# Performance work log

Hardware: AMD Instinct MI355X
Metric: run time of the kernel (lower is better)

Reference implementation:

```python
import jax, jax.numpy as jnp
import numpy as np

KERNEL_MUL = 2.0
KERNEL_NUM = 5


def setup_inputs() -> dict:
    key = jax.random.key(0)
    k1, k2 = jax.random.split(key)
    N, D = 4096, 256
    source = jax.random.normal(k1, (N, D), dtype=jnp.float32)
    target = jax.random.normal(k2, (N, D), dtype=jnp.float32)
    return {"source": source, "target": target}


def _gaussian_kernel_sum(source, target):
    # total: [2N, D]
    total = jnp.concatenate([source, target], axis=0)
    n = total.shape[0]
    sq = jnp.sum(total * total, axis=1)  # [2N]
    L2 = sq[:, None] + sq[None, :] - 2.0 * (total @ total.T)  # [2N, 2N]
    # Bandwidth from detached mean of off-diagonal-normalized sum (torch uses .data)
    bandwidth = jax.lax.stop_gradient(jnp.sum(L2)) / (n * n - n)
    bandwidth = bandwidth / (KERNEL_MUL ** (KERNEL_NUM // 2))
    kernels = sum(
        jnp.exp(-L2 / (bandwidth * (KERNEL_MUL ** i))) for i in range(KERNEL_NUM)
    )
    return kernels


def reference(source, target):
    b = source.shape[0]
    K = _gaussian_kernel_sum(source, target)
    XX = jnp.mean(K[:b, :b])
    YY = jnp.mean(K[b:, b:])
    XY = jnp.mean(K[:b, b:])
    YX = jnp.mean(K[b:, :b])
    return XX + YY - XY - YX
```

## Files before the change

kernel.cpp:

```cpp
#include <hip/hip_runtime.h>


#define NROWS 8192
#define HALF  4096
#define DIM   256
#define BM    128
#define CONVB 256
#define NTILE 2080

typedef __bf16 bf16x8 __attribute__((ext_vector_type(8)));
typedef float f32x4 __attribute__((ext_vector_type(4)));
typedef unsigned short ushort8 __attribute__((ext_vector_type(8)));

__device__ __forceinline__ const float* row_ptr(const float* src, const float* tgt, int r) {
    return (r < HALF) ? (src + (size_t)r * DIM) : (tgt + (size_t)(r - HALF) * DIM);
}

__device__ __forceinline__ unsigned short bf16_rne(float x) {
    unsigned int u = __builtin_bit_cast(unsigned int, x);
    return (unsigned short)((u + 0x7FFFu + ((u >> 16) & 1u)) >> 16);
}

__global__ __launch_bounds__(256) void k_conv(const float* __restrict__ src,
                                              const float* __restrict__ tgt,
                                              unsigned short* __restrict__ hi,
                                              float* __restrict__ sq,
                                              float* __restrict__ part,
                                              double* __restrict__ parts1,
                                              double* __restrict__ accum) {
    __shared__ __align__(16) unsigned short sh_hi[32 * 32 * 8];
    __shared__ float4 cs[4][64];
    __shared__ double s1s[4];

    int w = threadIdx.x >> 6, lane = threadIdx.x & 63;
    int r0 = blockIdx.x * 32;
    int g  = lane >> 1, j = lane & 1;
    float4 csum = {0.f, 0.f, 0.f, 0.f};
    double s1w = 0.0;
    #pragma unroll
    for (int i = 0; i < 8; ++i) {
        int rl  = w * 8 + i;
        int row = r0 + rl;
        const float* rp = row_ptr(src, tgt, row);
        float4 v = ((const float4*)rp)[lane];
        float xs[4] = {v.x, v.y, v.z, v.w};
        unsigned short hs[4];
        #pragma unroll
        for (int k = 0; k < 4; ++k) hs[k] = bf16_rne(xs[k]);
        ushort4 h4 = {hs[0], hs[1], hs[2], hs[3]};
        int so = (g * 32 + rl) * 8 + j * 4;
        *(ushort4*)&sh_hi[so] = h4;
        csum.x += v.x; csum.y += v.y; csum.z += v.z; csum.w += v.w;
        float s = v.x * v.x + v.y * v.y + v.z * v.z + v.w * v.w;
        #pragma unroll
        for (int off = 32; off; off >>= 1) s += __shfl_xor(s, off, 64);
        if (lane == 0) { sq[row] = s; s1w += (double)s; }
    }
    __syncthreads();
    int panel = blockIdx.x >> 2, quarter = blockIdx.x & 3;
    #pragma unroll
    for (int c = threadIdx.x; c < 1024; c += 256) {
        int gg = c >> 5, r = c & 31;
        size_t goff = (((size_t)panel * 32 + gg) * 128 + quarter * 32 + r) * 8;
        *(ushort8*)&hi[goff] = *(const ushort8*)&sh_hi[c * 8];
    }
    cs[w][lane] = csum;
    if (lane == 0) s1s[w] = s1w;
    __syncthreads();
    if (w == 0) {
        float4 a = cs[0][lane], b = cs[1][lane], c = cs[2][lane], d = cs[3][lane];
        float4 tot = {a.x + b.x + c.x + d.x, a.y + b.y + c.y + d.y,
                      a.z + b.z + c.z + d.z, a.w + b.w + c.w + d.w};
        *(float4*)&part[(size_t)blockIdx.x * DIM + lane * 4] = tot;
        if (lane == 0) parts1[blockIdx.x] = s1s[0] + s1s[1] + s1s[2] + s1s[3];
    }
    if (blockIdx.x == 0 && threadIdx.x == 0) *accum = 0.0;
}

__global__ __launch_bounds__(256) void k_scale(const double* __restrict__ parts1,
                                               const float* __restrict__ part,
                                               float* __restrict__ scale) {
    __shared__ double sh[256];
    int t = threadIdx.x;
    sh[t] = parts1[t];
    __syncthreads();
    for (int off = 128; off; off >>= 1) {
        if (t < off) sh[t] += sh[t + off];
        __syncthreads();
    }
    double S1 = sh[0];
    __syncthreads();
    float c0 = 0.f, c1 = 0.f, c2 = 0.f, c3 = 0.f;
    #pragma unroll 16
    for (int b = 0; b < CONVB; b += 4) {
        c0 += part[(b + 0) * DIM + t];
        c1 += part[(b + 1) * DIM + t];
        c2 += part[(b + 2) * DIM + t];
        c3 += part[(b + 3) * DIM + t];
    }
    double c = (double)((c0 + c1) + (c2 + c3));
    sh[t] = c * c;
    __syncthreads();
    for (int off = 128; off; off >>= 1) {
        if (t < off) sh[t] += sh[t + off];
        __syncthreads();
    }
    if (t == 0) {
        double S2    = sh[0];
        double n     = (double)NROWS;
        double sumL2 = 2.0 * n * S1 - 2.0 * S2;
        double bw    = sumL2 / (n * n - n) / 4.0;
        *scale = (float)(-1.0 / (16.0 * bw * 0.69314718055994530942));
    }
}

__global__ __launch_bounds__(256, 2) void k_pairs(const unsigned short* __restrict__ hi,
                                                  const float* __restrict__ sq,
                                                  const float* __restrict__ scale_p,
                                                  double* __restrict__ accum) {
    int gidx = blockIdx.x;
    int I = 0;
    for (;;) {
        int rowcnt = 36 + 64 * (7 - I);
        if (gidx < rowcnt) break;
        gidx -= rowcnt; ++I;
    }
    int bi, bj;
    if (gidx < 36) {
        int r = 0, c = gidx;
        while (c >= 8 - r) { c -= 8 - r; ++r; }
        bi = 8 * I + r; bj = 8 * I + r + c;
    } else {
        int o = gidx - 36;
        int J = I + 1 + (o >> 6);
        int k2 = o & 63;
        bi = 8 * I + (k2 >> 3); bj = 8 * J + (k2 & 7);
    }

    __shared__ float wsum[4];

    int t    = threadIdx.x;
    int lane = t & 63;
    int w    = t >> 6;
    int wr   = w >> 1, wc = w & 1;
    int lr   = lane & 15, lq = lane >> 4;
    int ro = bi * BM, co = bj * BM;

    size_t aBase = (size_t)bi * 4096 + lq * 128 + wr * 64 + lr;
    size_t bBase = (size_t)bj * 4096 + lq * 128 + wc * 64 + lr;
    const ushort8* pAh = (const ushort8*)hi + aBase;
    const ushort8* pBh = (const ushort8*)hi + bBase;

    f32x4 acc[4][4];
    #pragma unroll
    for (int m = 0; m < 4; ++m)
        #pragma unroll
        for (int n = 0; n < 4; ++n) acc[m][n] = (f32x4){0.f, 0.f, 0.f, 0.f};

    #pragma unroll
    for (int it = 0; it < DIM / 128; ++it) {
        bf16x8 aH[4][4], bH[4][4];
        #pragma unroll
        for (int h = 0; h < 4; ++h) {
            #pragma unroll
            for (int m = 0; m < 4; ++m) {
                aH[h][m] = __builtin_bit_cast(bf16x8, pAh[it * 2048 + h * 512 + m * 16]);
                bH[h][m] = __builtin_bit_cast(bf16x8, pBh[it * 2048 + h * 512 + m * 16]);
            }
        }
        #pragma unroll
        for (int h = 0; h < 4; ++h)
            #pragma unroll
            for (int m = 0; m < 4; ++m)
                #pragma unroll
                for (int n = 0; n < 4; ++n)
                    acc[m][n] = __builtin_amdgcn_mfma_f32_16x16x32_bf16(aH[h][m], bH[h][n], acc[m][n], 0, 0, 0);
    }

    float scale = *scale_p;
    int ro_eff = ro + wr * 64, co_eff = co + wc * 64;
    float4 sqa4[4];
    float  sqbv[4];
    #pragma unroll
    for (int m = 0; m < 4; ++m) sqa4[m] = *(const float4*)&sq[ro_eff + m * 16 + lq * 4];
    #pragma unroll
    for (int n = 0; n < 4; ++n) sqbv[n] = sq[co_eff + n * 16 + lr];

    float tsum = 0.0f;
    #pragma unroll
    for (int m = 0; m < 4; ++m) {
        float sa[4] = {sqa4[m].x, sqa4[m].y, sqa4[m].z, sqa4[m].w};
        #pragma unroll
        for (int n = 0; n < 4; ++n) {
            #pragma unroll
            for (int r = 0; r < 4; ++r) {
                float L2  = sa[r] + sqbv[n] - 2.0f * acc[m][n][r];
                float u   = __builtin_amdgcn_exp2f(scale * L2);
                float u2  = u * u;
                float u4  = u2 * u2;
                float u8  = u4 * u4;
                float u16 = u8 * u8;
                tsum += u + u2 + u4 + u8 + u16;
            }
        }
    }

    #pragma unroll
    for (int off = 32; off; off >>= 1) tsum += __shfl_xor(tsum, off, 64);
    if (lane == 0) wsum[w] = tsum;
    __syncthreads();
    if (t == 0) {
        float tot = wsum[0] + wsum[1] + wsum[2] + wsum[3];
        float sgn = ((ro < HALF) == (co < HALF)) ? 1.0f : -1.0f;
        float wgt = (bi == bj) ? 1.0f : 2.0f;
        atomicAdd(accum, (double)(sgn * wgt * tot));
    }
}

__global__ void k_fin(const double* __restrict__ accum, float* __restrict__ out) {
    out[0] = (float)(*accum / ((double)HALF * (double)HALF));
}

extern "C" void kernel_launch(void* const* d_in, const int* in_sizes, int n_in,
                              void* d_out, int out_size, void* d_ws, size_t ws_size,
                              hipStream_t stream) {
    const float* src = (const float*)d_in[0];
    const float* tgt = (const float*)d_in[1];
    float* out = (float*)d_out;

    char* ws = (char*)d_ws;
    double* accum  = (double*)ws;
    float*  scale  = (float*)(ws + 16);
    float*  sq     = (float*)(ws + 64);
    float*  part   = (float*)(ws + 64 + 32768);
    double* parts1 = (double*)(ws + 64 + 32768 + 262144);
    unsigned short* hi = (unsigned short*)(ws + 297024);

    k_conv <<<CONVB, 256, 0, stream>>>(src, tgt, hi, sq, part, parts1, accum);
    k_scale<<<1, 256, 0, stream>>>(parts1, part, scale);
    k_pairs<<<NTILE, 256, 0, stream>>>(hi, sq, scale, accum);
    k_fin  <<<1, 1, 0, stream>>>(accum, out);
}
```

Baseline: 112.7 us.

## Remap pair kernel to 256x128 blocks with per-wave 64x128 tiles

Replaces the 128x128 upper-triangle block tiling (2080 blocks) with blocks covering two 128-row panels against one 128-column panel (1056 blocks). Each wave now computes a 64x128 tile with 32 accumulators and loops over K in 32-wide steps, loading 4 A and 8 B fragments per step. The triangular weighting moves to per-wave weights of 0, 1 or 2, so some waves compute tiles that are then discarded. This aims to raise operand reuse per wave and cut block count, at the cost of more accumulator registers and some wasted work on diagonal blocks.

```diff
diff --git a/kernel.cpp b/kernel.cpp
--- a/kernel.cpp
+++ b/kernel.cpp
@@ -4,9 +4,8 @@
 #define NROWS 8192
 #define HALF  4096
 #define DIM   256
-#define BM    128
 #define CONVB 256
-#define NTILE 2080
+#define NTILE 1056
 
 typedef __bf16 bf16x8 __attribute__((ext_vector_type(8)));
 typedef float f32x4 __attribute__((ext_vector_type(4)));
@@ -118,80 +117,70 @@
                                                   const float* __restrict__ sq,
                                                   const float* __restrict__ scale_p,
                                                   double* __restrict__ accum) {
-    int gidx = blockIdx.x;
+    int id = blockIdx.x;
     int I = 0;
     for (;;) {
-        int rowcnt = 36 + 64 * (7 - I);
-        if (gidx < rowcnt) break;
-        gidx -= rowcnt; ++I;
-    }
-    int bi, bj;
-    if (gidx < 36) {
-        int r = 0, c = gidx;
-        while (c >= 8 - r) { c -= 8 - r; ++r; }
-        bi = 8 * I + r; bj = 8 * I + r + c;
-    } else {
-        int o = gidx - 36;
-        int J = I + 1 + (o >> 6);
-        int k2 = o & 63;
-        bi = 8 * I + (k2 >> 3); bj = 8 * J + (k2 & 7);
-    }
+        int cnt = 64 - 2 * I;
+        if (id < cnt) break;
+        id -= cnt; ++I;
+    }
+    int J = 2 * I + id;
 
     __shared__ float wsum[4];
 
     int t    = threadIdx.x;
     int lane = t & 63;
     int w    = t >> 6;
-    int wr   = w >> 1, wc = w & 1;
     int lr   = lane & 15, lq = lane >> 4;
-    int ro = bi * BM, co = bj * BM;
-
-    size_t aBase = (size_t)bi * 4096 + lq * 128 + wr * 64 + lr;
-    size_t bBase = (size_t)bj * 4096 + lq * 128 + wc * 64 + lr;
+    int Pw   = 2 * I + (w >> 1);
+    int hh   = w & 1;
+
+    float wgt = (J == Pw) ? 1.0f : (J > Pw) ? 2.0f : 0.0f;
+    float sgn = ((Pw < 32) == (J < 32)) ? 1.0f : -1.0f;
+
+    size_t aBase = (size_t)Pw * 4096 + lq * 128 + hh * 64 + lr;
+    size_t bBase = (size_t)J  * 4096 + lq * 128 + lr;
     const ushort8* pAh = (const ushort8*)hi + aBase;
     const ushort8* pBh = (const ushort8*)hi + bBase;
 
-    f32x4 acc[4][4];
+    f32x4 acc[4][8];
     #pragma unroll
     for (int m = 0; m < 4; ++m)
         #pragma unroll
-        for (int n = 0; n < 4; ++n) acc[m][n] = (f32x4){0.f, 0.f, 0.f, 0.f};
-
-    #pragma unroll
-    for (int it = 0; it < DIM / 128; ++it) {
-        bf16x8 aH[4][4], bH[4][4];
-        #pragma unroll
-        for (int h = 0; h < 4; ++h) {
+        for (int n = 0; n < 8; ++n) acc[m][n] = (f32x4){0.f, 0.f, 0.f, 0.f};
+
+    #pragma unroll
+    for (int it = 0; it < DIM / 32; ++it) {
+        bf16x8 aH[4], bH[8];
+        #pragma unroll
+        for (int m = 0; m < 4; ++m)
+            aH[m] = __builtin_bit_cast(bf16x8, pAh[it * 512 + m * 16]);
+        #pragma unroll
+        for (int n = 0; n < 8; ++n)
+            bH[n] = __builtin_bit_cast(bf16x8, pBh[it * 512 + n * 16]);
+        #pragma unroll
+        for (int m = 0; m < 4; ++m)
             #pragma unroll
-            for (int m = 0; m < 4; ++m) {
-                aH[h][m] = __builtin_bit_cast(bf16x8, pAh[it * 2048 + h * 512 + m * 16]);
-                bH[h][m] = __builtin_bit_cast(bf16x8, pBh[it * 2048 + h * 512 + m * 16]);
-            }
-        }
-        #pragma unroll
-        for (int h = 0; h < 4; ++h)
-            #pragma unroll
-            for (int m = 0; m < 4; ++m)
-                #pragma unroll
-                for (int n = 0; n < 4; ++n)
-                    acc[m][n] = __builtin_amdgcn_mfma_f32_16x16x32_bf16(aH[h][m], bH[h][n], acc[m][n], 0, 0, 0);
+            for (int n = 0; n < 8; ++n)
+                acc[m][n] = __builtin_amdgcn_mfma_f32_16x16x32_bf16(aH[m], bH[n], acc[m][n], 0, 0, 0);
     }
 
     float scale = *scale_p;
-    int ro_eff = ro + wr * 64, co_eff = co + wc * 64;
+    int ro_eff = Pw * 128 + hh * 64;
+    int co_eff = J * 128;
     float4 sqa4[4];
-    float  sqbv[4];
+    float  sqbv[8];
     #pragma unroll
     for (int m = 0; m < 4; ++m) sqa4[m] = *(const float4*)&sq[ro_eff + m * 16 + lq * 4];
     #pragma unroll
-    for (int n = 0; n < 4; ++n) sqbv[n] = sq[co_eff + n * 16 + lr];
+    for (int n = 0; n < 8; ++n) sqbv[n] = sq[co_eff + n * 16 + lr];
 
     float tsum = 0.0f;
     #pragma unroll
     for (int m = 0; m < 4; ++m) {
         float sa[4] = {sqa4[m].x, sqa4[m].y, sqa4[m].z, sqa4[m].w};
         #pragma unroll
-        for (int n = 0; n < 4; ++n) {
+        for (int n = 0; n < 8; ++n) {
             #pragma unroll
             for (int r = 0; r < 4; ++r) {
                 float L2  = sa[r] + sqbv[n] - 2.0f * acc[m][n][r];
@@ -207,13 +196,11 @@
 
     #pragma unroll
     for (int off = 32; off; off >>= 1) tsum += __shfl_xor(tsum, off, 64);
-    if (lane == 0) wsum[w] = tsum;
+    if (lane == 0) wsum[w] = tsum * sgn * wgt;
     __syncthreads();
     if (t == 0) {
         float tot = wsum[0] + wsum[1] + wsum[2] + wsum[3];
-        float sgn = ((ro < HALF) == (co < HALF)) ? 1.0f : -1.0f;
-        float wgt = (bi == bj) ? 1.0f : 2.0f;
-        atomicAdd(accum, (double)(sgn * wgt * tot));
+        atomicAdd(accum, (double)tot);
     }
 }
 
```

New measurement: 110.9 us. About the same (-1.6%).
